# Performance work log

Hardware: AMD Instinct MI355X
Metric: run time of the kernel (lower is better)

Reference implementation:

```python
import jax, jax.numpy as jnp
import numpy as np

N, C, H, W = 8, 21, 512, 512
POWER = 1
EPS = 1e-8

def setup_inputs() -> dict:
    key = jax.random.key(0)
    k1, k2 = jax.random.split(key)
    inp = jax.random.normal(k1, (N, C, H, W), dtype=jnp.float32)
    tgt = jax.random.normal(k2, (N, C, H, W), dtype=jnp.float32)
    return {"input": inp, "target": tgt}

def reference(input, target):
    n, c, h, w = input.shape
    # target.argmax(1) -> one-hot mask (to_one_hot with clamp; argmax already in [0, c-1])
    labels = jnp.argmax(target, axis=1)                      # [n, h, w]
    ymask = jax.nn.one_hot(labels, c, axis=1, dtype=input.dtype)  # [n, c, h, w]

    log_p = jax.nn.log_softmax(input, axis=1)
    p = jax.nn.softmax(input, axis=1)

    # lambda_mat is None -> zf_dict: lamb[i][j] = 0.5 for all i, j
    lamb = jnp.full((c, c), 0.5, dtype=input.dtype)

    # Per-class pixel counts n_i and pairwise sums S[i, j] = sum(p[:, i] * ymask[:, j])
    counts = ymask.sum(axis=(0, 2, 3))                       # [c]
    S = jnp.einsum('nihw,njhw->ij', p, ymask)                # [c, c]

    safe_counts = jnp.where(counts > 0, counts, 1.0)
    diag = jnp.diagonal(S)                                   # S[i, i]
    # mcc.sum() for pair (i, j) = S[i,i]/n_i - S[i,j]/n_j
    mcc_sum = diag[:, None] / safe_counts[:, None] - S / safe_counts[None, :]

    term = -lamb * jnp.log((0.5 * mcc_sum + 0.5) ** POWER + EPS)
    valid = (counts[:, None] > 0) & (counts[None, :] > 0) & (~jnp.eye(c, dtype=bool))
    lossd = jnp.where(valid, term, 0.0).sum()

    # weight is None -> ymask1 == ymask
    logpy = (log_p * ymask).sum(axis=1)                      # [n, h, w]
    loss = -logpy.mean()
    return loss + lossd
```

## Files before the change

### kernel.cpp

```cpp
#include <hip/hip_runtime.h>

#define BLOCK 256
#define GRID 2048

namespace {
constexpr int C = 21;
constexpr int HW = 512 * 512;
constexpr int NPIX = 8 * HW;
constexpr int CH4 = HW / 4;
constexpr float EPS = 1e-8f;
constexpr int WS_CNT = C * C;
constexpr int WS_LOGP = C * C + C;
constexpr int ACC_USED = C * C + C + 1;
constexpr int ACC_STRIDE = 464;
constexpr int MAX_COPIES = 64;
}

__global__ __launch_bounds__(BLOCK)
__attribute__((amdgpu_waves_per_eu(2, 2)))
void wce_main(const float* __restrict__ inp,
              const float* __restrict__ tgt,
              float* __restrict__ acc,
              int copy_mask) {
    __shared__ float sS[C * C];
    __shared__ float sCnt[C];
    __shared__ float sRed[BLOCK / 64];

    const int tid = threadIdx.x;
    for (int i = tid; i < C * C; i += BLOCK) sS[i] = 0.f;
    if (tid < C) sCnt[tid] = 0.f;
    __syncthreads();

    const int g = blockIdx.x * BLOCK + tid;
    const int pix0 = g << 2;
    const int n = pix0 >> 18;
    const int hw = pix0 & (HW - 1);
    const size_t base = (size_t)n * (size_t)(C * HW) + (size_t)hw;

    const float4* __restrict__ tp = reinterpret_cast<const float4*>(tgt + base);
    const float4* __restrict__ ip = reinterpret_cast<const float4*>(inp + base);

    float4 t[C], x[C];
#pragma unroll
    for (int c = 0; c < C; ++c) t[c] = tp[c * CH4];
#pragma unroll
    for (int c = 0; c < C; ++c) x[c] = ip[c * CH4];

    float4 bv = t[0];
    int bx = 0, by = 0, bz = 0, bw = 0;
#pragma unroll
    for (int c = 1; c < C; ++c) {
        if (t[c].x > bv.x) { bv.x = t[c].x; bx = c; }
        if (t[c].y > bv.y) { bv.y = t[c].y; by = c; }
        if (t[c].z > bv.z) { bv.z = t[c].z; bz = c; }
        if (t[c].w > bv.w) { bv.w = t[c].w; bw = c; }
    }

    float4 m = x[0];
#pragma unroll
    for (int c = 1; c < C; ++c) {
        m.x = fmaxf(m.x, x[c].x);
        m.y = fmaxf(m.y, x[c].y);
        m.z = fmaxf(m.z, x[c].z);
        m.w = fmaxf(m.w, x[c].w);
    }

    float4 xlab = x[0];
#pragma unroll
    for (int c = 1; c < C; ++c) {
        if (bx == c) xlab.x = x[c].x;
        if (by == c) xlab.y = x[c].y;
        if (bz == c) xlab.z = x[c].z;
        if (bw == c) xlab.w = x[c].w;
    }

    float4 s = make_float4(0.f, 0.f, 0.f, 0.f);
#pragma unroll
    for (int c = 0; c < C; ++c) {
        x[c].x = __expf(x[c].x - m.x); s.x += x[c].x;
        x[c].y = __expf(x[c].y - m.y); s.y += x[c].y;
        x[c].z = __expf(x[c].z - m.z); s.z += x[c].z;
        x[c].w = __expf(x[c].w - m.w); s.w += x[c].w;
    }

    float lp = (xlab.x - m.x - __logf(s.x))
             + (xlab.y - m.y - __logf(s.y))
             + (xlab.z - m.z - __logf(s.z))
             + (xlab.w - m.w - __logf(s.w));

    const float ix = 1.f / s.x, iy = 1.f / s.y, iz = 1.f / s.z, iw = 1.f / s.w;
#pragma unroll
    for (int c = 0; c < C; ++c) {
        unsafeAtomicAdd(&sS[c * C + bx], x[c].x * ix);
        unsafeAtomicAdd(&sS[c * C + by], x[c].y * iy);
        unsafeAtomicAdd(&sS[c * C + bz], x[c].z * iz);
        unsafeAtomicAdd(&sS[c * C + bw], x[c].w * iw);
    }
    unsafeAtomicAdd(&sCnt[bx], 1.f);
    unsafeAtomicAdd(&sCnt[by], 1.f);
    unsafeAtomicAdd(&sCnt[bz], 1.f);
    unsafeAtomicAdd(&sCnt[bw], 1.f);

#pragma unroll
    for (int off = 32; off > 0; off >>= 1) lp += __shfl_down(lp, off);
    if ((tid & 63) == 0) sRed[tid >> 6] = lp;
    __syncthreads();

    float* __restrict__ a = acc + (size_t)(blockIdx.x & copy_mask) * ACC_STRIDE;
    for (int i = tid; i < C * C; i += BLOCK) unsafeAtomicAdd(&a[i], sS[i]);
    if (tid < C) unsafeAtomicAdd(&a[WS_CNT + tid], sCnt[tid]);
    if (tid == 0) {
        float tt = 0.f;
#pragma unroll
        for (int wv = 0; wv < BLOCK / 64; ++wv) tt += sRed[wv];
        unsafeAtomicAdd(&a[WS_LOGP], tt);
    }
}

__global__ void wce_final(const float* __restrict__ acc, float* __restrict__ out,
                          int copies) {
    __shared__ float tot[ACC_USED];
    __shared__ float red[8];
    const int tid = threadIdx.x;

    for (int i = tid; i < ACC_USED; i += 512) {
        float s = 0.f;
        for (int k = 0; k < copies; ++k) s += acc[(size_t)k * ACC_STRIDE + i];
        tot[i] = s;
    }
    __syncthreads();

    float partial = 0.f;
    if (tid < C * C) {
        const int i = tid / C;
        const int j = tid - i * C;
        if (i != j) {
            const float ci = tot[WS_CNT + i], cj = tot[WS_CNT + j];
            if (ci > 0.f && cj > 0.f) {
                const float mcc = tot[i * C + i] / ci - tot[i * C + j] / cj;
                partial = -0.5f * __logf(0.5f * mcc + 0.5f + EPS);
            }
        }
    }
#pragma unroll
    for (int off = 32; off > 0; off >>= 1) partial += __shfl_down(partial, off);
    if ((tid & 63) == 0) red[tid >> 6] = partial;
    __syncthreads();

    if (tid == 0) {
        float lossd = 0.f;
#pragma unroll
        for (int wv = 0; wv < 8; ++wv) lossd += red[wv];
        const float loss = -tot[WS_LOGP] / (float)NPIX;
        out[0] = loss + lossd;
    }
}

extern "C" void kernel_launch(void* const* d_in, const int* in_sizes, int n_in,
                              void* d_out, int out_size, void* d_ws, size_t ws_size,
                              hipStream_t stream) {
    const float* inp = (const float*)d_in[0];
    const float* tgt = (const float*)d_in[1];
    float* acc = (float*)d_ws;
    float* out = (float*)d_out;

    int copies = 1;
    const size_t per = (size_t)ACC_STRIDE * sizeof(float);
    while (copies * 2 <= MAX_COPIES && (size_t)(copies * 2) * per <= ws_size) copies *= 2;

    hipMemsetAsync(acc, 0, (size_t)copies * per, stream);
    wce_main<<<GRID, BLOCK, 0, stream>>>(inp, tgt, acc, copies - 1);
    wce_final<<<1, 512, 0, stream>>>(acc, out, copies);
}
```

Baseline: 286.4 us.

## Stage channel tiles in LDS via direct global-to-LDS DMA loads

Replaces the per-thread register loading of all 21 channels of target and input with global_load_lds DMA into a shared tile, first for target (argmax) and then reusing the same buffer for input. The block size is halved and the grid doubled, and the register-heavy waves_per_eu constraint is dropped, to cut register pressure and allow more waves in flight. The exponentials are recomputed in the atomic pass instead of being kept in registers. This trades register usage for extra LDS reads, a second exp pass, and full vmcnt waits that serialize the two load phases within each block.

```diff
diff --git a/kernel.cpp b/kernel.cpp
--- a/kernel.cpp
+++ b/kernel.cpp
@@ -1,13 +1,13 @@
 #include <hip/hip_runtime.h>
 
-#define BLOCK 256
-#define GRID 2048
+#define BLOCK 128
+#define GRID 4096
 
 namespace {
 constexpr int C = 21;
 constexpr int HW = 512 * 512;
 constexpr int NPIX = 8 * HW;
-constexpr int CH4 = HW / 4;
+constexpr int PTILE = 512;
 constexpr float EPS = 1e-8f;
 constexpr int WS_CNT = C * C;
 constexpr int WS_LOGP = C * C + C;
@@ -16,71 +16,82 @@
 constexpr int MAX_COPIES = 64;
 }
 
-__global__ __launch_bounds__(BLOCK)
-__attribute__((amdgpu_waves_per_eu(2, 2)))
-void wce_main(const float* __restrict__ inp,
-              const float* __restrict__ tgt,
-              float* __restrict__ acc,
-              int copy_mask) {
+__device__ __forceinline__ void lds_dma16(const float* g, float* l) {
+    __builtin_amdgcn_global_load_lds(
+        (const __attribute__((address_space(1))) void*)g,
+        (__attribute__((address_space(3))) void*)l,
+        16, 0, 0);
+}
+
+__global__ __launch_bounds__(BLOCK) void wce_main(const float* __restrict__ inp,
+                                                  const float* __restrict__ tgt,
+                                                  float* __restrict__ acc,
+                                                  int copy_mask) {
+    __shared__ __align__(16) float buf[C][PTILE];
     __shared__ float sS[C * C];
     __shared__ float sCnt[C];
     __shared__ float sRed[BLOCK / 64];
 
     const int tid = threadIdx.x;
+    const int wid = tid >> 6;
+
     for (int i = tid; i < C * C; i += BLOCK) sS[i] = 0.f;
     if (tid < C) sCnt[tid] = 0.f;
+
+    const int px0 = blockIdx.x * PTILE;
+    const int n = px0 >> 18;
+    const int hw = px0 & (HW - 1);
+    const float* __restrict__ tbase = tgt + (size_t)n * (size_t)(C * HW) + hw;
+    const float* __restrict__ ibase = inp + (size_t)n * (size_t)(C * HW) + hw;
+    const int lane4 = tid * 4;
+
+#pragma unroll
+    for (int c = 0; c < C; ++c)
+        lds_dma16(tbase + (size_t)c * HW + lane4, &buf[c][wid * 256]);
+    asm volatile("s_waitcnt vmcnt(0)" ::: "memory");
     __syncthreads();
 
-    const int g = blockIdx.x * BLOCK + tid;
-    const int pix0 = g << 2;
-    const int n = pix0 >> 18;
-    const int hw = pix0 & (HW - 1);
-    const size_t base = (size_t)n * (size_t)(C * HW) + (size_t)hw;
-
-    const float4* __restrict__ tp = reinterpret_cast<const float4*>(tgt + base);
-    const float4* __restrict__ ip = reinterpret_cast<const float4*>(inp + base);
-
-    float4 t[C], x[C];
-#pragma unroll
-    for (int c = 0; c < C; ++c) t[c] = tp[c * CH4];
-#pragma unroll
-    for (int c = 0; c < C; ++c) x[c] = ip[c * CH4];
-
-    float4 bv = t[0];
+    float4 bv = reinterpret_cast<const float4*>(&buf[0][0])[tid];
     int bx = 0, by = 0, bz = 0, bw = 0;
 #pragma unroll
     for (int c = 1; c < C; ++c) {
-        if (t[c].x > bv.x) { bv.x = t[c].x; bx = c; }
-        if (t[c].y > bv.y) { bv.y = t[c].y; by = c; }
-        if (t[c].z > bv.z) { bv.z = t[c].z; bz = c; }
-        if (t[c].w > bv.w) { bv.w = t[c].w; bw = c; }
+        const float4 t = reinterpret_cast<const float4*>(&buf[c][0])[tid];
+        if (t.x > bv.x) { bv.x = t.x; bx = c; }
+        if (t.y > bv.y) { bv.y = t.y; by = c; }
+        if (t.z > bv.z) { bv.z = t.z; bz = c; }
+        if (t.w > bv.w) { bv.w = t.w; bw = c; }
     }
+    __syncthreads();
 
-    float4 m = x[0];
+#pragma unroll
+    for (int c = 0; c < C; ++c)
+        lds_dma16(ibase + (size_t)c * HW + lane4, &buf[c][wid * 256]);
+    asm volatile("s_waitcnt vmcnt(0)" ::: "memory");
+    __syncthreads();
+
+    float4 m = reinterpret_cast<const float4*>(&buf[0][0])[tid];
+    float4 xlab = m;
 #pragma unroll
     for (int c = 1; c < C; ++c) {
-        m.x = fmaxf(m.x, x[c].x);
-        m.y = fmaxf(m.y, x[c].y);
-        m.z = fmaxf(m.z, x[c].z);
-        m.w = fmaxf(m.w, x[c].w);
-    }
-
-    float4 xlab = x[0];
-#pragma unroll
-    for (int c = 1; c < C; ++c) {
-        if (bx == c) xlab.x = x[c].x;
-        if (by == c) xlab.y = x[c].y;
-        if (bz == c) xlab.z = x[c].z;
-        if (bw == c) xlab.w = x[c].w;
+        const float4 v = reinterpret_cast<const float4*>(&buf[c][0])[tid];
+        m.x = fmaxf(m.x, v.x);
+        m.y = fmaxf(m.y, v.y);
+        m.z = fmaxf(m.z, v.z);
+        m.w = fmaxf(m.w, v.w);
+        if (bx == c) xlab.x = v.x;
+        if (by == c) xlab.y = v.y;
+        if (bz == c) xlab.z = v.z;
+        if (bw == c) xlab.w = v.w;
     }
 
     float4 s = make_float4(0.f, 0.f, 0.f, 0.f);
 #pragma unroll
     for (int c = 0; c < C; ++c) {
-        x[c].x = __expf(x[c].x - m.x); s.x += x[c].x;
-        x[c].y = __expf(x[c].y - m.y); s.y += x[c].y;
-        x[c].z = __expf(x[c].z - m.z); s.z += x[c].z;
-        x[c].w = __expf(x[c].w - m.w); s.w += x[c].w;
+        const float4 v = reinterpret_cast<const float4*>(&buf[c][0])[tid];
+        s.x += __expf(v.x - m.x);
+        s.y += __expf(v.y - m.y);
+        s.z += __expf(v.z - m.z);
+        s.w += __expf(v.w - m.w);
     }
 
     float lp = (xlab.x - m.x - __logf(s.x))
@@ -91,10 +102,11 @@
     const float ix = 1.f / s.x, iy = 1.f / s.y, iz = 1.f / s.z, iw = 1.f / s.w;
 #pragma unroll
     for (int c = 0; c < C; ++c) {
-        unsafeAtomicAdd(&sS[c * C + bx], x[c].x * ix);
-        unsafeAtomicAdd(&sS[c * C + by], x[c].y * iy);
-        unsafeAtomicAdd(&sS[c * C + bz], x[c].z * iz);
-        unsafeAtomicAdd(&sS[c * C + bw], x[c].w * iw);
+        const float4 v = reinterpret_cast<const float4*>(&buf[c][0])[tid];
+        unsafeAtomicAdd(&sS[c * C + bx], __expf(v.x - m.x) * ix);
+        unsafeAtomicAdd(&sS[c * C + by], __expf(v.y - m.y) * iy);
+        unsafeAtomicAdd(&sS[c * C + bz], __expf(v.z - m.z) * iz);
+        unsafeAtomicAdd(&sS[c * C + bw], __expf(v.w - m.w) * iw);
     }
     unsafeAtomicAdd(&sCnt[bx], 1.f);
     unsafeAtomicAdd(&sCnt[by], 1.f);
@@ -103,7 +115,7 @@
 
 #pragma unroll
     for (int off = 32; off > 0; off >>= 1) lp += __shfl_down(lp, off);
-    if ((tid & 63) == 0) sRed[tid >> 6] = lp;
+    if ((tid & 63) == 0) sRed[wid] = lp;
     __syncthreads();
 
     float* __restrict__ a = acc + (size_t)(blockIdx.x & copy_mask) * ACC_STRIDE;
```

Result: slower. 307.2 us (+7.3%).
